# Performance work log

Measured on AMD Instinct MI355X. Metric: run time of the kernel, lower is better.

The kernel has to match this reference:

```python
import jax, jax.numpy as jnp
import numpy as np

B, H, S, DK = 4, 16, 2048, 64


def setup_inputs() -> dict:
    key = jax.random.key(0)
    kq, kk, kv, km = jax.random.split(key, 4)
    Q = jax.random.normal(kq, (B, H, S, DK), dtype=jnp.float32)
    K = jax.random.normal(kk, (B, H, S, DK), dtype=jnp.float32)
    V = jax.random.normal(kv, (B, H, S, DK), dtype=jnp.float32)
    mask = (jax.random.uniform(km, (B, 1, S, S)) > 0.1).astype(jnp.float32)
    return {"Q": Q, "K": K, "V": V, "mask": mask}


def reference(Q, K, V, mask):
    d_k = Q.shape[-1]
    # unnormalized exp scores (no max subtraction), multiplicative mask
    scores = jnp.exp(jnp.einsum("bhqd,bhkd->bhqk", Q, K) / jnp.sqrt(jnp.float32(d_k)))
    scores = scores * mask
    attn = scores / (jnp.sum(scores, axis=-1, keepdims=True) + 1e-8)
    return jnp.einsum("bhqk,bhkd->bhqd", attn, V)
```

## Files before the change

### kernel.cpp

```cpp
#include <hip/hip_runtime.h>

namespace {
constexpr int S  = 2048;
constexpr int D  = 64;
constexpr int BQ = 128;
constexpr int BK = 64;
constexpr int NT = 256;
constexpr int NKT = S / BK;

typedef short bf16x8 __attribute__((ext_vector_type(8)));
typedef float f32x4  __attribute__((ext_vector_type(4)));

__device__ inline unsigned short bf16c(float x) {
  __bf16 h = (__bf16)x;
  return __builtin_bit_cast(unsigned short, h);
}
__device__ inline unsigned pk2(float a, float b) {
  return (unsigned)bf16c(a) | ((unsigned)bf16c(b) << 16);
}
__device__ inline void gld_lds16(const void* g, void* l) {
  __builtin_amdgcn_global_load_lds(
      (const __attribute__((address_space(1))) unsigned int*)g,
      (__attribute__((address_space(3))) unsigned int*)l, 16, 0, 0);
}
#if __has_builtin(__builtin_amdgcn_exp2f)
__device__ inline float exp2v(float x) { return __builtin_amdgcn_exp2f(x); }
#else
__device__ inline float exp2v(float x) { return __expf(x * 0.6931471805599453f); }
#endif

__device__ inline int kswz_of_row(int row) {
  return (row & 3) | (((row >> 3) & 1) << 2);
}

__device__ inline bf16x8 mk_pa(f32x4 s0, f32x4 s1, unsigned mw0, unsigned mw1) {
  uint4 u;
  u.x = pk2(exp2v(s0[0]), exp2v(s0[1])) & __builtin_amdgcn_perm(0u, mw0, 0x01010000u);
  u.y = pk2(exp2v(s0[2]), exp2v(s0[3])) & __builtin_amdgcn_perm(0u, mw0, 0x03030202u);
  u.z = pk2(exp2v(s1[0]), exp2v(s1[1])) & __builtin_amdgcn_perm(0u, mw1, 0x01010000u);
  u.w = pk2(exp2v(s1[2]), exp2v(s1[3])) & __builtin_amdgcn_perm(0u, mw1, 0x03030202u);
  return __builtin_bit_cast(bf16x8, u);
}

__global__ __launch_bounds__(256) void prep_k(const float* __restrict__ K,
                                              unsigned short* __restrict__ Kws) {
  int gid = blockIdx.x * 256 + threadIdx.x;
  int row = gid >> 3;
  int g   = gid & 7;
  const float* src = K + (size_t)row * 64 + g * 8;
  float4 a = *(const float4*)src;
  float4 b = *(const float4*)(src + 4);
  uint4 w;
  w.x = pk2(a.x, a.y); w.y = pk2(a.z, a.w);
  w.z = pk2(b.x, b.y); w.w = pk2(b.z, b.w);
  *(uint4*)(Kws + (size_t)row * 64 + ((g ^ kswz_of_row(row)) * 8)) = w;
}

__global__ __launch_bounds__(512) void prep_v(const float* __restrict__ V,
                                              unsigned short* __restrict__ Vws) {
  __shared__ __align__(16) unsigned char smem[51200];
  const int t    = threadIdx.x;
  const int half = t >> 8;
  const int tsub = t & 255;
  const size_t tile = (size_t)blockIdx.x * 2 + half;
  float* tl = (float*)smem + half * (64 * 68);
  unsigned short* so = (unsigned short*)(smem + 34816) + half * 4096;
  const float* src = V + tile * (64 * 64);
#pragma unroll
  for (int rep = 0; rep < 4; ++rep) {
    int idx = tsub + rep * 256;
    int row = idx >> 4, d4 = idx & 15;
    float4 v = *(const float4*)(src + row * 64 + d4 * 4);
    *(float4*)(tl + row * 68 + d4 * 4) = v;
  }
  __syncthreads();
#pragma unroll
  for (int rep = 0; rep < 2; ++rep) {
    int d  = (tsub & 31) + rep * 32;
    int kg = tsub >> 5;
    float x[8];
#pragma unroll
    for (int j = 0; j < 8; ++j) x[j] = tl[(kg * 8 + j) * 68 + d];
    uint4 w;
    w.x = pk2(x[0], x[1]); w.y = pk2(x[2], x[3]);
    w.z = pk2(x[4], x[5]); w.w = pk2(x[6], x[7]);
    *(uint4*)(so + d * 64 + ((kg ^ (d & 7)) * 8)) = w;
  }
  __syncthreads();
  unsigned short* dstT = Vws + tile * (64 * 64);
#pragma unroll
  for (int rep = 0; rep < 2; ++rep) {
    int i = tsub + rep * 256;
    *(uint4*)(dstT + i * 8) = *(const uint4*)(so + i * 8);
  }
}

__global__ __launch_bounds__(512) void prep_m(const float* __restrict__ M,
                                              unsigned char* __restrict__ M2) {
  __shared__ unsigned nibs[32][129];
  const int t  = threadIdx.x;
  const int b  = blockIdx.x >> 6;
  const int qg = blockIdx.x & 63;
  const float* src = M + ((size_t)b * S + (size_t)qg * 32) * S;
#pragma unroll
  for (int pass = 0; pass < 8; ++pass) {
    int idx = pass * 512 + t;
    int q  = idx >> 7;
    int kc = idx & 127;
    const float* p = src + (size_t)q * S + kc * 16;
    unsigned w = 0;
#pragma unroll
    for (int j = 0; j < 4; ++j) {
      float4 v = *(const float4*)(p + j * 4);
      unsigned nib = (v.x != 0.f ? 1u : 0u) | (v.y != 0.f ? 2u : 0u) |
                     (v.z != 0.f ? 4u : 0u) | (v.w != 0.f ? 8u : 0u);
      w |= nib << (8 * j);
    }
    nibs[q][kc] = w;
  }
  __syncthreads();
  const int e    = t & 127;
  const int lane = e >> 1, g = e & 1;
  const int n16  = lane & 15, quad = lane >> 4;
  const int qq   = g * 16 + n16;
  const int c    = quad >> 1;
  const int sh0  = 8 * ((2 * quad) & 3);
  unsigned char* dstb = M2 + ((size_t)b * NKT * 64 + qg) * 2048 + (size_t)e * 16;
#pragma unroll
  for (int i = 0; i < 8; ++i) {
    int kt = (t >> 7) + i * 4;
    unsigned d0 = nibs[qq][kt * 4 + c];
    unsigned d1 = nibs[qq][kt * 4 + 2 + c];
    unsigned n00 = (d0 >> sh0) & 0xFu;
    unsigned n01 = (d0 >> (sh0 + 8)) & 0xFu;
    unsigned n10 = (d1 >> sh0) & 0xFu;
    unsigned n11 = (d1 >> (sh0 + 8)) & 0xFu;
    uint4 out;
    out.x = ((n00 * 0x00204081u) & 0x01010101u) * 255u;
    out.y = ((n01 * 0x00204081u) & 0x01010101u) * 255u;
    out.z = ((n10 * 0x00204081u) & 0x01010101u) * 255u;
    out.w = ((n11 * 0x00204081u) & 0x01010101u) * 255u;
    *(uint4*)(dstb + (size_t)kt * (64 * 64 * 32)) = out;
  }
}

__global__ __launch_bounds__(NT, 4)
void attn3(const float* __restrict__ Qg, const unsigned char* __restrict__ M2,
           const unsigned short* __restrict__ Kws,
           const unsigned short* __restrict__ Vws,
           float* __restrict__ Og) {
  __shared__ __align__(16) unsigned short sK[2][BK * D];
  __shared__ __align__(16) unsigned short sV[2][BK * D];

  const int t    = threadIdx.x;
  const int wave = t >> 6;
  const int lane = t & 63;
  const int quad = lane >> 4;
  const int n16  = lane & 15;

  const int bh = blockIdx.y;
  const int b  = bh >> 4;
  const int q0 = blockIdx.x * BQ;
  const int qg = blockIdx.x * 4 + wave;

  const unsigned short* Kb = Kws + (size_t)bh * S * D;
  const unsigned short* Vb = Vws + (size_t)bh * S * D;
  const unsigned char* Mp = M2 + (((size_t)b * NKT * 64 + qg) * 64 + lane) * 32;
  constexpr size_t MKT = (size_t)64 * 64 * 32;

  const int h2 = n16 >> 2, rr = n16 & 3;
  const int krow0 = (8 * h2 + rr) * 64;

  const int sw = n16 & 7;
  const int ga = (quad ^ sw) * 8;
  const int gb = ((quad + 4) ^ sw) * 8;

  constexpr float QS = 0.18033688011112042f;
  const float* QbA = Qg + ((size_t)bh * S + q0 + wave * 32 + n16) * D;
  bf16x8 aqA[2], aqB[2];
#pragma unroll
  for (int ks = 0; ks < 2; ++ks) {
    const float* qp = QbA + ks * 32 + quad * 8;
    float4 x = *(const float4*)qp;
    float4 y = *(const float4*)(qp + 4);
    bf16x8 a;
    a[0] = (short)bf16c(x.x * QS); a[1] = (short)bf16c(x.y * QS);
    a[2] = (short)bf16c(x.z * QS); a[3] = (short)bf16c(x.w * QS);
    a[4] = (short)bf16c(y.x * QS); a[5] = (short)bf16c(y.y * QS);
    a[6] = (short)bf16c(y.z * QS); a[7] = (short)bf16c(y.w * QS);
    aqA[ks] = a;
    const float* qp2 = qp + 16 * D;
    float4 x2 = *(const float4*)qp2;
    float4 y2 = *(const float4*)(qp2 + 4);
    bf16x8 a2;
    a2[0] = (short)bf16c(x2.x * QS); a2[1] = (short)bf16c(x2.y * QS);
    a2[2] = (short)bf16c(x2.z * QS); a2[3] = (short)bf16c(x2.w * QS);
    a2[4] = (short)bf16c(y2.x * QS); a2[5] = (short)bf16c(y2.y * QS);
    a2[6] = (short)bf16c(y2.z * QS); a2[7] = (short)bf16c(y2.w * QS);
    aqB[ks] = a2;
  }

  bf16x8 ones;
#pragma unroll
  for (int i = 0; i < 8; ++i) ones[i] = (short)0x3F80;

  f32x4 oA[4], oB[4];
#pragma unroll
  for (int nt = 0; nt < 4; ++nt) {
    oA[nt] = (f32x4){0.f, 0.f, 0.f, 0.f};
    oB[nt] = (f32x4){0.f, 0.f, 0.f, 0.f};
  }
  f32x4 rsA = (f32x4){0.f, 0.f, 0.f, 0.f};
  f32x4 rsB = (f32x4){0.f, 0.f, 0.f, 0.f};

  gld_lds16(Kb + wave * 512 + lane * 8, &sK[0][wave * 512]);
  gld_lds16(Kb + 2048 + wave * 512 + lane * 8, &sK[0][2048 + wave * 512]);
  gld_lds16(Vb + wave * 512 + lane * 8, &sV[0][wave * 512]);
  gld_lds16(Vb + 2048 + wave * 512 + lane * 8, &sV[0][2048 + wave * 512]);
  uint4 mkA[2], mkB[2];
  mkA[0] = *(const uint4*)Mp;
  mkB[0] = *(const uint4*)(Mp + 16);

#pragma unroll 2
  for (int kt = 0; kt < NKT; ++kt) {
    const int cur = kt & 1, nxt = cur ^ 1;
    __syncthreads();

    if (kt + 1 < NKT) {
      const size_t gbase = (size_t)(kt + 1) * (BK * D);
      gld_lds16(Kb + gbase + wave * 512 + lane * 8, &sK[nxt][wave * 512]);
      gld_lds16(Kb + gbase + 2048 + wave * 512 + lane * 8,
                &sK[nxt][2048 + wave * 512]);
      gld_lds16(Vb + gbase + wave * 512 + lane * 8, &sV[nxt][wave * 512]);
      gld_lds16(Vb + gbase + 2048 + wave * 512 + lane * 8,
                &sV[nxt][2048 + wave * 512]);
      mkA[nxt] = *(const uint4*)(Mp + (size_t)(kt + 1) * MKT);
      mkB[nxt] = *(const uint4*)(Mp + (size_t)(kt + 1) * MKT + 16);
    }

    bf16x8 paA[2], paB[2];
#pragma unroll
    for (int ks = 0; ks < 2; ++ks) {
      const unsigned short* base = &sK[cur][krow0 + ks * 2048];
      bf16x8 k0a = *(const bf16x8*)(base + ga);
      bf16x8 k0b = *(const bf16x8*)(base + gb);
      bf16x8 k1a = *(const bf16x8*)(base + 256 + ga);
      bf16x8 k1b = *(const bf16x8*)(base + 256 + gb);
      const f32x4 z = (f32x4){0.f, 0.f, 0.f, 0.f};

      f32x4 sA0 = __builtin_amdgcn_mfma_f32_16x16x32_bf16(k0a, aqA[0], z, 0, 0, 0);
      sA0 = __builtin_amdgcn_mfma_f32_16x16x32_bf16(k0b, aqA[1], sA0, 0, 0, 0);
      f32x4 sA1 = __builtin_amdgcn_mfma_f32_16x16x32_bf16(k1a, aqA[0], z, 0, 0, 0);
      sA1 = __builtin_amdgcn_mfma_f32_16x16x32_bf16(k1b, aqA[1], sA1, 0, 0, 0);
      paA[ks] = mk_pa(sA0, sA1, ks ? mkA[cur].z : mkA[cur].x,
                                ks ? mkA[cur].w : mkA[cur].y);

      f32x4 sB0 = __builtin_amdgcn_mfma_f32_16x16x32_bf16(k0a, aqB[0], z, 0, 0, 0);
      sB0 = __builtin_amdgcn_mfma_f32_16x16x32_bf16(k0b, aqB[1], sB0, 0, 0, 0);
      f32x4 sB1 = __builtin_amdgcn_mfma_f32_16x16x32_bf16(k1a, aqB[0], z, 0, 0, 0);
      sB1 = __builtin_amdgcn_mfma_f32_16x16x32_bf16(k1b, aqB[1], sB1, 0, 0, 0);
      paB[ks] = mk_pa(sB0, sB1, ks ? mkB[cur].z : mkB[cur].x,
                                ks ? mkB[cur].w : mkB[cur].y);
    }

    rsA = __builtin_amdgcn_mfma_f32_16x16x32_bf16(ones, paA[0], rsA, 0, 0, 0);
    rsA = __builtin_amdgcn_mfma_f32_16x16x32_bf16(ones, paA[1], rsA, 0, 0, 0);
    rsB = __builtin_amdgcn_mfma_f32_16x16x32_bf16(ones, paB[0], rsB, 0, 0, 0);
    rsB = __builtin_amdgcn_mfma_f32_16x16x32_bf16(ones, paB[1], rsB, 0, 0, 0);

#pragma unroll
    for (int nt = 0; nt < 4; ++nt) {
      const int row = nt * 16 + n16;
      bf16x8 v0 = *(const bf16x8*)(sV[cur] + row * 64 + ga);
      bf16x8 v1 = *(const bf16x8*)(sV[cur] + row * 64 + gb);
      oA[nt] = __builtin_amdgcn_mfma_f32_16x16x32_bf16(v0, paA[0], oA[nt], 0, 0, 0);
      oA[nt] = __builtin_amdgcn_mfma_f32_16x16x32_bf16(v1, paA[1], oA[nt], 0, 0, 0);
      oB[nt] = __builtin_amdgcn_mfma_f32_16x16x32_bf16(v0, paB[0], oB[nt], 0, 0, 0);
      oB[nt] = __builtin_amdgcn_mfma_f32_16x16x32_bf16(v1, paB[1], oB[nt], 0, 0, 0);
    }
  }

  const float invA = 1.0f / (rsA[0] + 1e-8f);
  const float invB = 1.0f / (rsB[0] + 1e-8f);
  float* OA = Og + ((size_t)bh * S + q0 + wave * 32 + n16) * D;
#pragma unroll
  for (int nt = 0; nt < 4; ++nt) {
    float4 wa = make_float4(oA[nt][0] * invA, oA[nt][1] * invA,
                            oA[nt][2] * invA, oA[nt][3] * invA);
    *(float4*)(OA + nt * 16 + quad * 4) = wa;
    float4 wb = make_float4(oB[nt][0] * invB, oB[nt][1] * invB,
                            oB[nt][2] * invB, oB[nt][3] * invB);
    *(float4*)(OA + 16 * D + nt * 16 + quad * 4) = wb;
  }
}
}

extern "C" void kernel_launch(void* const* d_in, const int* in_sizes, int n_in,
                              void* d_out, int out_size, void* d_ws, size_t ws_size,
                              hipStream_t stream) {
  const float* Q = (const float*)d_in[0];
  const float* K = (const float*)d_in[1];
  const float* V = (const float*)d_in[2];
  const float* M = (const float*)d_in[3];
  float* O = (float*)d_out;

  unsigned short* Kws = (unsigned short*)d_ws;
  unsigned short* Vws = Kws + (size_t)64 * S * D;
  unsigned char*  M2  = (unsigned char*)(Vws + (size_t)64 * S * D);

  prep_k<<<dim3(64 * S * D / 8 / 256), 256, 0, stream>>>(K, Kws);
  prep_v<<<dim3(64 * NKT / 2), 512, 0, stream>>>(V, Vws);
  prep_m<<<dim3(4 * 64), 512, 0, stream>>>(M, M2);
  attn3<<<dim3(S / BQ, 64), NT, 0, stream>>>(Q, M2, Kws, Vws, O);
}
```

Baseline: 269.5 us.

## Drop mask prepass and read fp32 mask directly inside attention kernel

Removes the prep_m kernel, which packed the fp32 mask into byte masks laid out per MFMA lane. The attention kernel now loads fp32 mask values straight from global memory each K tile and multiplies them into the exp scores. This saves one kernel launch and one full pass over the 64 MB mask. In exchange each attention block rereads fp32 mask rows, 16 times across heads, relying on L2/MALL hits. The mask loads are also no longer prefetched one tile ahead.

Result: slower. 324.5 us (+20.4%).

```diff
diff --git a/kernel.cpp b/kernel.cpp
--- a/kernel.cpp
+++ b/kernel.cpp
@@ -33,12 +33,12 @@
   return (row & 3) | (((row >> 3) & 1) << 2);
 }
 
-__device__ inline bf16x8 mk_pa(f32x4 s0, f32x4 s1, unsigned mw0, unsigned mw1) {
+__device__ inline bf16x8 mk_pa(f32x4 s0, f32x4 s1, float4 m0, float4 m1) {
   uint4 u;
-  u.x = pk2(exp2v(s0[0]), exp2v(s0[1])) & __builtin_amdgcn_perm(0u, mw0, 0x01010000u);
-  u.y = pk2(exp2v(s0[2]), exp2v(s0[3])) & __builtin_amdgcn_perm(0u, mw0, 0x03030202u);
-  u.z = pk2(exp2v(s1[0]), exp2v(s1[1])) & __builtin_amdgcn_perm(0u, mw1, 0x01010000u);
-  u.w = pk2(exp2v(s1[2]), exp2v(s1[3])) & __builtin_amdgcn_perm(0u, mw1, 0x03030202u);
+  u.x = pk2(exp2v(s0[0]) * m0.x, exp2v(s0[1]) * m0.y);
+  u.y = pk2(exp2v(s0[2]) * m0.z, exp2v(s0[3]) * m0.w);
+  u.z = pk2(exp2v(s1[0]) * m1.x, exp2v(s1[1]) * m1.y);
+  u.w = pk2(exp2v(s1[2]) * m1.z, exp2v(s1[3]) * m1.w);
   return __builtin_bit_cast(bf16x8, u);
 }
 
@@ -95,57 +95,8 @@
   }
 }
 
-__global__ __launch_bounds__(512) void prep_m(const float* __restrict__ M,
-                                              unsigned char* __restrict__ M2) {
-  __shared__ unsigned nibs[32][129];
-  const int t  = threadIdx.x;
-  const int b  = blockIdx.x >> 6;
-  const int qg = blockIdx.x & 63;
-  const float* src = M + ((size_t)b * S + (size_t)qg * 32) * S;
-#pragma unroll
-  for (int pass = 0; pass < 8; ++pass) {
-    int idx = pass * 512 + t;
-    int q  = idx >> 7;
-    int kc = idx & 127;
-    const float* p = src + (size_t)q * S + kc * 16;
-    unsigned w = 0;
-#pragma unroll
-    for (int j = 0; j < 4; ++j) {
-      float4 v = *(const float4*)(p + j * 4);
-      unsigned nib = (v.x != 0.f ? 1u : 0u) | (v.y != 0.f ? 2u : 0u) |
-                     (v.z != 0.f ? 4u : 0u) | (v.w != 0.f ? 8u : 0u);
-      w |= nib << (8 * j);
-    }
-    nibs[q][kc] = w;
-  }
-  __syncthreads();
-  const int e    = t & 127;
-  const int lane = e >> 1, g = e & 1;
-  const int n16  = lane & 15, quad = lane >> 4;
-  const int qq   = g * 16 + n16;
-  const int c    = quad >> 1;
-  const int sh0  = 8 * ((2 * quad) & 3);
-  unsigned char* dstb = M2 + ((size_t)b * NKT * 64 + qg) * 2048 + (size_t)e * 16;
-#pragma unroll
-  for (int i = 0; i < 8; ++i) {
-    int kt = (t >> 7) + i * 4;
-    unsigned d0 = nibs[qq][kt * 4 + c];
-    unsigned d1 = nibs[qq][kt * 4 + 2 + c];
-    unsigned n00 = (d0 >> sh0) & 0xFu;
-    unsigned n01 = (d0 >> (sh0 + 8)) & 0xFu;
-    unsigned n10 = (d1 >> sh0) & 0xFu;
-    unsigned n11 = (d1 >> (sh0 + 8)) & 0xFu;
-    uint4 out;
-    out.x = ((n00 * 0x00204081u) & 0x01010101u) * 255u;
-    out.y = ((n01 * 0x00204081u) & 0x01010101u) * 255u;
-    out.z = ((n10 * 0x00204081u) & 0x01010101u) * 255u;
-    out.w = ((n11 * 0x00204081u) & 0x01010101u) * 255u;
-    *(uint4*)(dstb + (size_t)kt * (64 * 64 * 32)) = out;
-  }
-}
-
 __global__ __launch_bounds__(NT, 4)
-void attn3(const float* __restrict__ Qg, const unsigned char* __restrict__ M2,
+void attn3(const float* __restrict__ Qg, const float* __restrict__ Mg,
            const unsigned short* __restrict__ Kws,
            const unsigned short* __restrict__ Vws,
            float* __restrict__ Og) {
@@ -161,12 +112,12 @@
   const int bh = blockIdx.y;
   const int b  = bh >> 4;
   const int q0 = blockIdx.x * BQ;
-  const int qg = blockIdx.x * 4 + wave;
 
   const unsigned short* Kb = Kws + (size_t)bh * S * D;
   const unsigned short* Vb = Vws + (size_t)bh * S * D;
-  const unsigned char* Mp = M2 + (((size_t)b * NKT * 64 + qg) * 64 + lane) * 32;
-  constexpr size_t MKT = (size_t)64 * 64 * 32;
+
+  const float* MrA = Mg + ((size_t)b * S + (size_t)(q0 + wave * 32 + n16)) * S;
+  const float* MrB = MrA + (size_t)16 * S;
 
   const int h2 = n16 >> 2, rr = n16 & 3;
   const int krow0 = (8 * h2 + rr) * 64;
@@ -217,9 +168,6 @@
   gld_lds16(Kb + 2048 + wave * 512 + lane * 8, &sK[0][2048 + wave * 512]);
   gld_lds16(Vb + wave * 512 + lane * 8, &sV[0][wave * 512]);
   gld_lds16(Vb + 2048 + wave * 512 + lane * 8, &sV[0][2048 + wave * 512]);
-  uint4 mkA[2], mkB[2];
-  mkA[0] = *(const uint4*)Mp;
-  mkB[0] = *(const uint4*)(Mp + 16);
 
 #pragma unroll 2
   for (int kt = 0; kt < NKT; ++kt) {
@@ -234,9 +182,17 @@
       gld_lds16(Vb + gbase + wave * 512 + lane * 8, &sV[nxt][wave * 512]);
       gld_lds16(Vb + gbase + 2048 + wave * 512 + lane * 8,
                 &sV[nxt][2048 + wave * 512]);
-      mkA[nxt] = *(const uint4*)(Mp + (size_t)(kt + 1) * MKT);
-      mkB[nxt] = *(const uint4*)(Mp + (size_t)(kt + 1) * MKT + 16);
     }
+
+    const int kb = kt * 64 + quad * 8;
+    float4 mA00 = *(const float4*)(MrA + kb);
+    float4 mA01 = *(const float4*)(MrA + kb + 4);
+    float4 mA10 = *(const float4*)(MrA + kb + 32);
+    float4 mA11 = *(const float4*)(MrA + kb + 36);
+    float4 mB00 = *(const float4*)(MrB + kb);
+    float4 mB01 = *(const float4*)(MrB + kb + 4);
+    float4 mB10 = *(const float4*)(MrB + kb + 32);
+    float4 mB11 = *(const float4*)(MrB + kb + 36);
 
     bf16x8 paA[2], paB[2];
 #pragma unroll
@@ -252,15 +208,13 @@
       sA0 = __builtin_amdgcn_mfma_f32_16x16x32_bf16(k0b, aqA[1], sA0, 0, 0, 0);
       f32x4 sA1 = __builtin_amdgcn_mfma_f32_16x16x32_bf16(k1a, aqA[0], z, 0, 0, 0);
       sA1 = __builtin_amdgcn_mfma_f32_16x16x32_bf16(k1b, aqA[1], sA1, 0, 0, 0);
-      paA[ks] = mk_pa(sA0, sA1, ks ? mkA[cur].z : mkA[cur].x,
-                                ks ? mkA[cur].w : mkA[cur].y);
+      paA[ks] = mk_pa(sA0, sA1, ks ? mA10 : mA00, ks ? mA11 : mA01);
 
       f32x4 sB0 = __builtin_amdgcn_mfma_f32_16x16x32_bf16(k0a, aqB[0], z, 0, 0, 0);
       sB0 = __builtin_amdgcn_mfma_f32_16x16x32_bf16(k0b, aqB[1], sB0, 0, 0, 0);
       f32x4 sB1 = __builtin_amdgcn_mfma_f32_16x16x32_bf16(k1a, aqB[0], z, 0, 0, 0);
       sB1 = __builtin_amdgcn_mfma_f32_16x16x32_bf16(k1b, aqB[1], sB1, 0, 0, 0);
-      paB[ks] = mk_pa(sB0, sB1, ks ? mkB[cur].z : mkB[cur].x,
-                                ks ? mkB[cur].w : mkB[cur].y);
+      paB[ks] = mk_pa(sB0, sB1, ks ? mB10 : mB00, ks ? mB11 : mB01);
     }
 
     rsA = __builtin_amdgcn_mfma_f32_16x16x32_bf16(ones, paA[0], rsA, 0, 0, 0);
@@ -306,10 +260,8 @@
 
   unsigned short* Kws = (unsigned short*)d_ws;
   unsigned short* Vws = Kws + (size_t)64 * S * D;
-  unsigned char*  M2  = (unsigned char*)(Vws + (size_t)64 * S * D);
 
   prep_k<<<dim3(64 * S * D / 8 / 256), 256, 0, stream>>>(K, Kws);
   prep_v<<<dim3(64 * NKT / 2), 512, 0, stream>>>(V, Vws);
-  prep_m<<<dim3(4 * 64), 512, 0, stream>>>(M, M2);
-  attn3<<<dim3(S / BQ, 64), NT, 0, stream>>>(Q, M2, Kws, Vws, O);
-}
+  attn3<<<dim3(S / BQ, 64), NT, 0, stream>>>(Q, M, Kws, Vws, O);
+}
```
